# Performance work log

Measured on AMD Instinct MI355X. Metric: run time of the kernel, lower is better.

The kernel has to match this reference:

```python
import jax, jax.numpy as jnp
import numpy as np

B, S, DIM, COV = 64, 512, 1024, 256


def setup_inputs() -> dict:
    key = jax.random.key(0)
    ks = jax.random.split(key, 12)
    s = 0.02
    h = jax.random.normal(ks[0], (B, DIM), jnp.float32)
    context = jax.random.normal(ks[1], (B, S, DIM), jnp.float32)
    cov = jax.random.normal(ks[2], (B, S, COV), jnp.float32)
    mask = jax.random.randint(ks[3], (B, S), 0, 2) == 1
    W_in = jax.random.normal(ks[4], (DIM, DIM), jnp.float32) * s
    W_out = jax.random.normal(ks[5], (DIM, 2 * DIM), jnp.float32) * s
    W_cov = jax.random.normal(ks[6], (DIM, COV), jnp.float32) * s
    b_cov = jax.random.normal(ks[7], (DIM,), jnp.float32) * s
    w_ih = jax.random.normal(ks[8], (3 * COV, 2 * DIM + 1), jnp.float32) * s
    w_hh = jax.random.normal(ks[9], (3 * COV, COV), jnp.float32) * s
    b_ih = jax.random.normal(ks[10], (3 * COV,), jnp.float32) * s
    b_hh = jax.random.normal(ks[11], (3 * COV,), jnp.float32) * s
    return dict(h=h, context=context, cov=cov, W_in=W_in, W_out=W_out,
                W_cov=W_cov, b_cov=b_cov, w_ih=w_ih, w_hh=w_hh,
                b_ih=b_ih, b_hh=b_hh, mask=mask)


def reference(h, context, cov, W_in, W_out, W_cov, b_cov, w_ih, w_hh, b_ih, b_hh, mask):
    # coverage-adjusted context: context + cov_linear(cov)  [B,S,DIM]
    ctx = context + jnp.einsum('bsc,dc->bsd', cov, W_cov) + b_cov
    # target = linear_in(h)  [B,DIM]
    target = h @ W_in.T
    # scores = bmm(context, target).squeeze(2)  [B,S]
    attn = jnp.einsum('bsd,bd->bs', ctx, target)
    attn = jnp.where(mask, -jnp.inf, attn)
    attn = jax.nn.softmax(attn, axis=1)
    # weighted_context = bmm(attn3, context)  [B,DIM]
    wc = jnp.einsum('bs,bsd->bd', attn, ctx)
    h_tilde = jnp.tanh(jnp.concatenate([wc, h], axis=1) @ W_out.T)
    # single-step GRU coverage update over B*S rows
    h_exp = jnp.broadcast_to(h[:, None, :], (B, S, DIM))
    x = jnp.concatenate([ctx, h_exp, attn[..., None]], axis=-1).reshape(B * S, 2 * DIM + 1)
    h0 = cov.reshape(B * S, COV)
    gx = x @ w_ih.T + b_ih   # [B*S, 3*COV]
    gh = h0 @ w_hh.T + b_hh  # [B*S, 3*COV]
    xr, xz, xn = jnp.split(gx, 3, axis=1)
    hr, hz, hn = jnp.split(gh, 3, axis=1)
    r = jax.nn.sigmoid(xr + hr)
    z = jax.nn.sigmoid(xz + hz)
    n = jnp.tanh(xn + r * hn)
    new_cov = ((1.0 - z) * n + z * h0).reshape(B, S, COV)
    return h_tilde, attn, new_cov
```

## Files before the change

kernel.cpp:

```cpp
#include <hip/hip_runtime.h>
#include <math.h>

typedef unsigned short ushort_t;
typedef __attribute__((ext_vector_type(8))) short short8;
typedef __attribute__((ext_vector_type(4))) float f32x4;
typedef __attribute__((ext_vector_type(4))) unsigned short ushort4v;

constexpr int B_ = 64, S_ = 512, DIM_ = 1024, COV_ = 256, TC_ = 768, KIH_ = 2049;
constexpr int NG_ = 1024, KG_ = 1280;

__device__ __forceinline__ float b2f(ushort_t u) {
    union { unsigned int i; float f; } v; v.i = ((unsigned int)u) << 16; return v.f;
}
__device__ __forceinline__ ushort_t f2b(float f) {
    unsigned int x = __float_as_uint(f);
    unsigned int r = x + 0x7fffu + ((x >> 16) & 1u);
    return (ushort_t)(r >> 16);
}
__device__ __forceinline__ float ldv(const float* p, size_t i) { return p[i]; }
__device__ __forceinline__ float ldv(const ushort_t* p, size_t i) { return b2f(p[i]); }

__device__ __forceinline__ float wave_reduce(float a) {
#pragma unroll
    for (int off = 32; off >= 1; off >>= 1) a += __shfl_down(a, off, 64);
    return a;
}

__device__ __forceinline__ void xpose4(f32x4& v, int l) {
    float s, r;
    s = (l & 1) ? v[0] : v[1]; r = __shfl_xor(s, 1, 64); if (l & 1) v[0] = r; else v[1] = r;
    s = (l & 1) ? v[2] : v[3]; r = __shfl_xor(s, 1, 64); if (l & 1) v[2] = r; else v[3] = r;
    s = (l & 2) ? v[0] : v[2]; r = __shfl_xor(s, 2, 64); if (l & 2) v[0] = r; else v[2] = r;
    s = (l & 2) ? v[1] : v[3]; r = __shfl_xor(s, 2, 64); if (l & 2) v[1] = r; else v[3] = r;
}

__global__ void k_detect(const unsigned char* __restrict__ mask,
                         const ushort_t* __restrict__ win,
                         int* __restrict__ flags) {
    __shared__ int red0[256];
    __shared__ int red1[256];
    int tid = threadIdx.x, mb = 0, f32 = 0;
    for (int i = tid; i < 32768; i += 256)
        if ((i & 3) != 0 && mask[i] != 0) mb = 1;
    for (int i = tid; i < 32768; i += 256) {
        ushort_t u = win[2 * i];
        if ((u & 0x7F80u) >= 0x4480u) f32 = 1;
    }
    red0[tid] = mb; red1[tid] = f32; __syncthreads();
    for (int st = 128; st >= 1; st >>= 1) {
        if (tid < st) { red0[tid] |= red0[tid + st]; red1[tid] |= red1[tid + st]; }
        __syncthreads();
    }
    if (tid == 0) { flags[0] = red0[0]; flags[1] = red1[0]; }
}

template <typename IT>
__device__ __forceinline__ void transpose_body(const IT* __restrict__ in,
                                               ushort_t* __restrict__ out,
                                               int R, int C, int ld, int off) {
    int idx = blockIdx.x * 256 + threadIdx.x;
    if (idx >= R * C) return;
    int r = idx / C, c = idx - r * C;
    out[c * R + r] = f2b(ldv(in, (size_t)r * ld + off + c));
}
__global__ void k_transpose(const void* __restrict__ in, ushort_t* __restrict__ out,
                            int R, int C, int ld, int off, const int* __restrict__ flags) {
    if (flags[1]) transpose_body((const float*)in, out, R, C, ld, off);
    else transpose_body((const ushort_t*)in, out, R, C, ld, off);
}

template <typename IT>
__device__ __forceinline__ void watt_body(const IT* __restrict__ wih, float* __restrict__ watt) {
    int j = threadIdx.x;
    watt[j] = ldv(wih, (size_t)j * KIH_ + 2048);
}
__global__ void k_watt(const void* __restrict__ wih, float* __restrict__ watt,
                       const int* __restrict__ flags) {
    if (flags[1]) watt_body((const float*)wih, watt);
    else watt_body((const ushort_t*)wih, watt);
}

template <typename IT>
__device__ __forceinline__ void bfold_body(const IT* __restrict__ bcov,
                                           const IT* __restrict__ wih,
                                           float* __restrict__ bfold) {
    int j = blockIdx.x * 4 + (threadIdx.x >> 6);
    int lane = threadIdx.x & 63;
    const IT* wr = wih + (size_t)j * KIH_;
    float a = 0.f;
#pragma unroll
    for (int i = 0; i < 16; ++i) { int k = lane + 64 * i; a += ldv(bcov, k) * ldv(wr, k); }
    a = wave_reduce(a);
    if (lane == 0) bfold[j] = a;
}
__global__ __launch_bounds__(256) void k_bfold(const void* __restrict__ bcov,
                                               const void* __restrict__ wih,
                                               float* __restrict__ bfold,
                                               const int* __restrict__ flags) {
    if (flags[1]) bfold_body((const float*)bcov, (const float*)wih, bfold);
    else bfold_body((const ushort_t*)bcov, (const ushort_t*)wih, bfold);
}

__global__ __launch_bounds__(256) void k_wfold(const ushort_t* __restrict__ wcov_t,
                                               const ushort_t* __restrict__ w_t,
                                               float* __restrict__ wfold) {
    __shared__ float col[DIM_];
    int c = blockIdx.x, tid = threadIdx.x;
    for (int d = tid; d < DIM_; d += 256) col[d] = b2f(wcov_t[c * DIM_ + d]);
    __syncthreads();
    float a0 = 0.f, a1 = 0.f, a2 = 0.f;
    for (int d = 0; d < DIM_; ++d) {
        float x = col[d];
        const ushort_t* wr = w_t + d * TC_;
        a0 += x * b2f(wr[tid]);
        a1 += x * b2f(wr[tid + 256]);
        a2 += x * b2f(wr[tid + 512]);
    }
    wfold[c * TC_ + tid] = a0;
    wfold[c * TC_ + tid + 256] = a1;
    wfold[c * TC_ + tid + 512] = a2;
}

template <typename IT>
__device__ __forceinline__ void buildwg_body(const IT* __restrict__ wih,
                                             const IT* __restrict__ whh,
                                             const float* __restrict__ wfold,
                                             ushort_t* __restrict__ wg) {
    int idx = blockIdx.x * 256 + threadIdx.x;
    if (idx >= NG_ * KG_) return;
    int n = idx / KG_, k = idx - n * KG_;
    int g = n & 3, cq = n >> 2;
    int j = g * COV_ + cq;
    float v;
    if (k < DIM_) {
        v = (j < TC_) ? ldv(wih, (size_t)j * KIH_ + k) : 0.f;
    } else {
        int c = k - DIM_;
        if (j < 512)      v = wfold[c * TC_ + j] + ldv(whh, (size_t)j * COV_ + c);
        else if (j < TC_) v = wfold[c * TC_ + j];
        else              v = ldv(whh, (size_t)(j - 256) * COV_ + c);
    }
    wg[(size_t)n * KG_ + k] = f2b(v);
}
__global__ void k_buildwg(const void* __restrict__ wih, const void* __restrict__ whh,
                          const float* __restrict__ wfold, ushort_t* __restrict__ wg,
                          const int* __restrict__ flags) {
    if (flags[1]) buildwg_body((const float*)wih, (const float*)whh, wfold, wg);
    else buildwg_body((const ushort_t*)wih, (const ushort_t*)whh, wfold, wg);
}

template <typename IT>
__device__ __forceinline__ void target_body(const IT* __restrict__ h,
                                            const IT* __restrict__ W_in,
                                            float* __restrict__ target) {
    int o = blockIdx.x * 4 + (threadIdx.x >> 6);
    int lane = threadIdx.x & 63;
    int b = o >> 10, d = o & (DIM_ - 1);
    const IT* hr = h + (size_t)b * DIM_;
    const IT* wr = W_in + (size_t)d * DIM_;
    float a = 0.f;
#pragma unroll
    for (int j = 0; j < 16; ++j) { int k = lane + 64 * j; a += ldv(hr, k) * ldv(wr, k); }
    a = wave_reduce(a);
    if (lane == 0) target[o] = a;
}
__global__ __launch_bounds__(256) void k_target_w(const void* __restrict__ h,
                                                  const void* __restrict__ W_in,
                                                  float* __restrict__ target,
                                                  const int* __restrict__ flags) {
    if (flags[1]) target_body((const float*)h, (const float*)W_in, target);
    else target_body((const ushort_t*)h, (const ushort_t*)W_in, target);
}

template <typename IT>
__device__ __forceinline__ void mvec_body(const float* __restrict__ target,
                                          const IT* __restrict__ W_cov,
                                          const IT* __restrict__ bcov,
                                          float* __restrict__ mvec,
                                          float* __restrict__ bct) {
    __shared__ float tg[DIM_];
    __shared__ float red[256];
    int b = blockIdx.x, tid = threadIdx.x;
    float pb = 0.f;
    for (int k = tid; k < DIM_; k += 256) {
        float t = target[b * DIM_ + k];
        tg[k] = t; pb += t * ldv(bcov, k);
    }
    red[tid] = pb; __syncthreads();
    for (int st = 128; st >= 1; st >>= 1) {
        if (tid < st) red[tid] += red[tid + st];
        __syncthreads();
    }
    float acc = 0.f;
    for (int d = 0; d < DIM_; ++d) acc += tg[d] * ldv(W_cov, (size_t)d * COV_ + tid);
    mvec[b * COV_ + tid] = acc;
    if (tid == 0) bct[b] = red[0];
}
__global__ __launch_bounds__(256) void k_mvec(const float* __restrict__ target,
                                              const void* __restrict__ W_cov,
                                              const void* __restrict__ bcov,
                                              float* __restrict__ mvec,
                                              float* __restrict__ bct,
                                              const int* __restrict__ flags) {
    if (flags[1]) mvec_body(target, (const float*)W_cov, (const float*)bcov, mvec, bct);
    else mvec_body(target, (const ushort_t*)W_cov, (const ushort_t*)bcov, mvec, bct);
}

template <typename IT>
__device__ __forceinline__ void scoreraw_body(const IT* __restrict__ context,
                                              const IT* __restrict__ cov,
                                              const float* __restrict__ target,
                                              const float* __restrict__ mvec,
                                              const float* __restrict__ bct,
                                              float* __restrict__ scf,
                                              ushort_t* __restrict__ ctx_bf,
                                              ushort_t* __restrict__ cov_bf) {
    __shared__ float tg[DIM_];
    __shared__ float ms[COV_];
    int b = blockIdx.x, tid = threadIdx.x;
    for (int k = tid; k < DIM_; k += 256) tg[k] = target[b * DIM_ + k];
    if (tid < COV_) ms[tid] = mvec[b * COV_ + tid];
    float bc = bct[b];
    __syncthreads();
    int wave = tid >> 6, lane = tid & 63;
    int s0 = blockIdx.y * 64 + wave * 16;
    for (int i = 0; i < 16; ++i) {
        int s = s0 + i;
        size_t row = (size_t)(b * S_ + s);
        const IT* cr = context + row * DIM_;
        const IT* vr = cov + row * COV_;
        float a = 0.f;
        if constexpr (sizeof(IT) == 4) {
#pragma unroll
            for (int j = 0; j < 4; ++j) {
                int d = lane * 4 + 256 * j;
                float4 x = *(const float4*)((const float*)cr + d);
                a += x.x * tg[d] + x.y * tg[d + 1] + x.z * tg[d + 2] + x.w * tg[d + 3];
                if (ctx_bf) {
                    ushort4v u;
                    u[0] = f2b(x.x); u[1] = f2b(x.y); u[2] = f2b(x.z); u[3] = f2b(x.w);
                    *(ushort4v*)(ctx_bf + row * DIM_ + d) = u;
                }
            }
            {
                int cc = lane * 4;
                float4 x = *(const float4*)((const float*)vr + cc);
                a += x.x * ms[cc] + x.y * ms[cc + 1] + x.z * ms[cc + 2] + x.w * ms[cc + 3];
                if (cov_bf) {
                    ushort4v u;
                    u[0] = f2b(x.x); u[1] = f2b(x.y); u[2] = f2b(x.z); u[3] = f2b(x.w);
                    *(ushort4v*)(cov_bf + row * COV_ + cc) = u;
                }
            }
        } else {
#pragma unroll
            for (int j = 0; j < 16; ++j) { int d = lane + 64 * j; a += ldv(cr, d) * tg[d]; }
#pragma unroll
            for (int j = 0; j < 4; ++j) { int c = lane + 64 * j; a += ldv(vr, c) * ms[c]; }
        }
        a = wave_reduce(a);
        if (lane == 0) scf[row] = a + bc;
    }
}
__global__ __launch_bounds__(256) void k_scoreraw(const void* __restrict__ context,
                                                  const void* __restrict__ cov,
                                                  const float* __restrict__ target,
                                                  const float* __restrict__ mvec,
                                                  const float* __restrict__ bct,
                                                  float* __restrict__ scf,
                                                  ushort_t* __restrict__ ctx_bf,
                                                  ushort_t* __restrict__ cov_bf,
                                                  const int* __restrict__ flags) {
    if (flags[1]) scoreraw_body((const float*)context, (const float*)cov, target, mvec, bct,
                                scf, ctx_bf, cov_bf);
    else scoreraw_body((const ushort_t*)context, (const ushort_t*)cov, target, mvec, bct,
                       scf, ctx_bf, cov_bf);
}

__global__ __launch_bounds__(256) void k_softmax(const float* __restrict__ scf,
                                                 const void* __restrict__ maskp,
                                                 const int* __restrict__ flags,
                                                 float* __restrict__ attnf,
                                                 float* __restrict__ attn_out) {
    __shared__ float red[256];
    int b = blockIdx.x, tid = threadIdx.x;
    int mb = flags[0];
    int i0 = b * S_ + tid, i1 = i0 + 256;
    int m0 = mb ? (int)((const unsigned char*)maskp)[i0] : ((const int*)maskp)[i0];
    int m1 = mb ? (int)((const unsigned char*)maskp)[i1] : ((const int*)maskp)[i1];
    float s0 = m0 ? -INFINITY : scf[i0];
    float s1 = m1 ? -INFINITY : scf[i1];
    red[tid] = fmaxf(s0, s1); __syncthreads();
    for (int st = 128; st >= 1; st >>= 1) {
        if (tid < st) red[tid] = fmaxf(red[tid], red[tid + st]);
        __syncthreads();
    }
    float mx = red[0]; __syncthreads();
    float e0 = expf(s0 - mx), e1 = expf(s1 - mx);
    red[tid] = e0 + e1; __syncthreads();
    for (int st = 128; st >= 1; st >>= 1) {
        if (tid < st) red[tid] += red[tid + st];
        __syncthreads();
    }
    float inv = 1.0f / red[0];
    float a0 = e0 * inv, a1 = e1 * inv;
    attnf[i0] = a0; attnf[i1] = a1;
    attn_out[i0] = a0; attn_out[i1] = a1;
}

__global__ __launch_bounds__(256) void k_wcpart2(const ushort_t* __restrict__ ctx_bf,
                                                 const ushort_t* __restrict__ cov_bf,
                                                 const void* __restrict__ ctx_in,
                                                 const void* __restrict__ cov_in,
                                                 const float* __restrict__ attnf,
                                                 float* __restrict__ wc8,
                                                 float* __restrict__ ac8,
                                                 const int* __restrict__ flags) {
    const ushort_t* C = flags[1] ? ctx_bf : (const ushort_t*)ctx_in;
    const ushort_t* V = flags[1] ? cov_bf : (const ushort_t*)cov_in;
    __shared__ float at[64];
    int b = blockIdx.x, ch = blockIdx.y, tid = threadIdx.x;
    int s0 = ch * 64;
    if (tid < 64) at[tid] = attnf[b * S_ + s0 + tid];
    __syncthreads();
    float acv = 0.f;
    for (int s = 0; s < 64; ++s)
        acv += at[s] * b2f(V[((size_t)(b * S_ + s0 + s)) * COV_ + tid]);
    ac8[((size_t)ch * B_ + b) * COV_ + tid] = acv;
    float acc[4] = {0.f, 0.f, 0.f, 0.f};
    for (int s = 0; s < 64; ++s) {
        float w = at[s];
        const ushort_t* cr = C + ((size_t)(b * S_ + s0 + s)) * DIM_;
        acc[0] += w * b2f(cr[tid]);
        acc[1] += w * b2f(cr[tid + 256]);
        acc[2] += w * b2f(cr[tid + 512]);
        acc[3] += w * b2f(cr[tid + 768]);
    }
    size_t base = ((size_t)ch * B_ + b) * DIM_;
    for (int m = 0; m < 4; ++m) wc8[base + tid + 256 * m] = acc[m];
}

template <typename IT>
__device__ __forceinline__ void wcfin_body(const float* __restrict__ wc8,
                                           const float* __restrict__ ac8,
                                           const ushort_t* __restrict__ wcov_t,
                                           const IT* __restrict__ bcov,
                                           float* __restrict__ wc) {
    __shared__ float ac[COV_];
    int b = blockIdx.x, tid = threadIdx.x;
    float a = 0.f;
    for (int ch = 0; ch < 8; ++ch) a += ac8[((size_t)ch * B_ + b) * COV_ + tid];
    ac[tid] = a;
    __syncthreads();
    float acc[4] = {0.f, 0.f, 0.f, 0.f};
    for (int ch = 0; ch < 8; ++ch) {
        size_t base = ((size_t)ch * B_ + b) * DIM_;
        for (int m = 0; m < 4; ++m) acc[m] += wc8[base + tid + 256 * m];
    }
    for (int c = 0; c < COV_; ++c) {
        float av = ac[c];
        const ushort_t* wr = wcov_t + c * DIM_;
        acc[0] += av * b2f(wr[tid]);
        acc[1] += av * b2f(wr[tid + 256]);
        acc[2] += av * b2f(wr[tid + 512]);
        acc[3] += av * b2f(wr[tid + 768]);
    }
    for (int m = 0; m < 4; ++m) {
        int d = tid + 256 * m;
        wc[b * DIM_ + d] = acc[m] + ldv(bcov, d);
    }
}
__global__ __launch_bounds__(256) void k_wcfin(const float* __restrict__ wc8,
                                               const float* __restrict__ ac8,
                                               const ushort_t* __restrict__ wcov_t,
                                               const void* __restrict__ bcov,
                                               float* __restrict__ wc,
                                               const int* __restrict__ flags) {
    if (flags[1]) wcfin_body(wc8, ac8, wcov_t, (const float*)bcov, wc);
    else wcfin_body(wc8, ac8, wcov_t, (const ushort_t*)bcov, wc);
}

template <typename IT>
__device__ __forceinline__ void htilde_body(const float* __restrict__ wc,
                                            const IT* __restrict__ h,
                                            const IT* __restrict__ W_out,
                                            float* __restrict__ out_ht) {
    int o = blockIdx.x * 4 + (threadIdx.x >> 6);
    int lane = threadIdx.x & 63;
    int b = o >> 10, d = o & (DIM_ - 1);
    const float* wcr = wc + b * DIM_;
    const IT* hr = h + (size_t)b * DIM_;
    const IT* wr = W_out + (size_t)d * 2 * DIM_;
    float a = 0.f;
#pragma unroll
    for (int j = 0; j < 16; ++j) { int k = lane + 64 * j; a += wcr[k] * ldv(wr, k); }
#pragma unroll
    for (int j = 0; j < 16; ++j) { int k = lane + 64 * j; a += ldv(hr, k) * ldv(wr, DIM_ + k); }
    a = wave_reduce(a);
    if (lane == 0) out_ht[o] = tanhf(a);
}
__global__ __launch_bounds__(256) void k_htilde_w(const float* __restrict__ wc,
                                                  const void* __restrict__ h,
                                                  const void* __restrict__ W_out,
                                                  float* __restrict__ out_ht,
                                                  const int* __restrict__ flags) {
    if (flags[1]) htilde_body(wc, (const float*)h, (const float*)W_out, out_ht);
    else htilde_body(wc, (const ushort_t*)h, (const ushort_t*)W_out, out_ht);
}

template <typename IT>
__device__ __forceinline__ void gxh_body(const IT* __restrict__ h,
                                         const IT* __restrict__ w_ih,
                                         const IT* __restrict__ b_ih,
                                         const float* __restrict__ bfold,
                                         float* __restrict__ gxall) {
    int o = blockIdx.x * 4 + (threadIdx.x >> 6);
    int lane = threadIdx.x & 63;
    int b = o / TC_, j = o - b * TC_;
    const IT* hr = h + (size_t)b * DIM_;
    const IT* wr = w_ih + (size_t)j * KIH_ + DIM_;
    float a = 0.f;
#pragma unroll
    for (int i = 0; i < 16; ++i) { int k = lane + 64 * i; a += ldv(hr, k) * ldv(wr, k); }
    a = wave_reduce(a);
    if (lane == 0) gxall[o] = a + ldv(b_ih, j) + bfold[j];
}
__global__ __launch_bounds__(256) void k_gxh_w(const void* __restrict__ h,
                                               const void* __restrict__ w_ih,
                                               const void* __restrict__ b_ih,
                                               const float* __restrict__ bfold,
                                               float* __restrict__ gxall,
                                               const int* __restrict__ flags) {
    if (flags[1]) gxh_body((const float*)h, (const float*)w_ih, (const float*)b_ih, bfold, gxall);
    else gxh_body((const ushort_t*)h, (const ushort_t*)w_ih, (const ushort_t*)b_ih, bfold, gxall);
}

__global__ __launch_bounds__(256) void k_gemm3(const ushort_t* __restrict__ ctx_bf,
                                               const ushort_t* __restrict__ cov_bf,
                                               const void* __restrict__ ctx_in,
                                               const void* __restrict__ cov_in,
                                               const ushort_t* __restrict__ wg,
                                               const float* __restrict__ attnf,
                                               const float* __restrict__ gxall,
                                               const float* __restrict__ watt,
                                               const void* __restrict__ bhh,
                                               float* __restrict__ out_cov,
                                               const int* __restrict__ flags) {
    const int f32in = flags[1];
    const ushort_t* Xc = f32in ? ctx_bf : (const ushort_t*)ctx_in;
    const ushort_t* Xv = f32in ? cov_bf : (const ushort_t*)cov_in;
    __shared__ __align__(16) ushort_t As[128 * 32];
    __shared__ __align__(16) ushort_t Bs[128 * 32];
    int tid = threadIdx.x;
    int p = blockIdx.x;
    int xcd = p & 7, t = p >> 3;
    int nb = t & 7, rb = xcd + 8 * (t >> 3);
    int n0 = nb * 128;
    int grow0 = rb * 128;
    int wave = tid >> 6, lane = tid & 63;
    int wm = wave >> 1, wn = wave & 1;
    int half = lane >> 4, r16 = lane & 15;

    int c0 = wave * 128 + lane;
    int ra0 = (c0) >> 2, sa0 = ((c0) & 3) ^ ((ra0 >> 1) & 3);
    int c1 = c0 + 64;
    int ra1 = (c1) >> 2, sa1 = ((c1) & 3) ^ ((ra1 >> 1) & 3);

    f32x4 acc[4][4];
#pragma unroll
    for (int i = 0; i < 4; ++i)
#pragma unroll
        for (int j = 0; j < 4; ++j) acc[i][j] = (f32x4){0.f, 0.f, 0.f, 0.f};

    for (int kt = 0; kt < KG_ / 32; ++kt) {
        int k0 = kt * 32;
        const ushort_t* X; size_t ldx; int kk0;
        if (k0 < DIM_) { X = Xc; ldx = DIM_; kk0 = k0; }
        else           { X = Xv; ldx = COV_; kk0 = k0 - DIM_; }
        {
            const ushort_t* g0 = X + (size_t)(grow0 + ra0) * ldx + kk0 + sa0 * 8;
            const ushort_t* g1 = X + (size_t)(grow0 + ra1) * ldx + kk0 + sa1 * 8;
            __builtin_amdgcn_global_load_lds(
                (const __attribute__((address_space(1))) void*)g0,
                (__attribute__((address_space(3))) void*)(As + (size_t)(wave * 128) * 8), 16, 0, 0);
            __builtin_amdgcn_global_load_lds(
                (const __attribute__((address_space(1))) void*)g1,
                (__attribute__((address_space(3))) void*)(As + (size_t)(wave * 128 + 64) * 8), 16, 0, 0);
        }
        {
            const ushort_t* g0 = wg + (size_t)(n0 + ra0) * KG_ + k0 + sa0 * 8;
            const ushort_t* g1 = wg + (size_t)(n0 + ra1) * KG_ + k0 + sa1 * 8;
            __builtin_amdgcn_global_load_lds(
                (const __attribute__((address_space(1))) void*)g0,
                (__attribute__((address_space(3))) void*)(Bs + (size_t)(wave * 128) * 8), 16, 0, 0);
            __builtin_amdgcn_global_load_lds(
                (const __attribute__((address_space(1))) void*)g1,
                (__attribute__((address_space(3))) void*)(Bs + (size_t)(wave * 128 + 64) * 8), 16, 0, 0);
        }
        __syncthreads();
        short8 a[4], b[4];
#pragma unroll
        for (int u = 0; u < 4; ++u) {
            int row = wm * 64 + u * 16 + r16;
            int sec = half ^ ((row >> 1) & 3);
            a[u] = *(const short8*)&As[row * 32 + sec * 8];
        }
#pragma unroll
        for (int u = 0; u < 4; ++u) {
            int row = wn * 64 + u * 16 + r16;
            int sec = half ^ ((row >> 1) & 3);
            b[u] = *(const short8*)&Bs[row * 32 + sec * 8];
        }
#pragma unroll
        for (int i = 0; i < 4; ++i)
#pragma unroll
            for (int j = 0; j < 4; ++j)
                acc[i][j] = __builtin_amdgcn_mfma_f32_16x16x32_bf16(a[i], b[j], acc[i][j], 0, 0, 0);
        __syncthreads();
    }

    int l = lane;
    int bb = grow0 >> 9;
    const float* gx = gxall + bb * TC_;
    int rowv[4]; float atv[4];
#pragma unroll
    for (int i = 0; i < 4; ++i) {
        rowv[i] = grow0 + wm * 64 + 16 * i + ((l >> 4) << 2) + (l & 3);
        atv[i] = attnf[rowv[i]];
    }
#pragma unroll
    for (int j = 0; j < 4; ++j) {
        int c = (n0 >> 2) + wn * 16 + 4 * j + ((l >> 2) & 3);
        float gxR = gx[c], gxZ = gx[COV_ + c], gxN = gx[2 * COV_ + c];
        float waR = watt[c], waZ = watt[COV_ + c], waN = watt[2 * COV_ + c];
        float bhR, bhZ, bhN;
        if (f32in) {
            const float* bp = (const float*)bhh;
            bhR = bp[c]; bhZ = bp[COV_ + c]; bhN = bp[2 * COV_ + c];
        } else {
            const ushort_t* bp = (const ushort_t*)bhh;
            bhR = b2f(bp[c]); bhZ = b2f(bp[COV_ + c]); bhN = b2f(bp[2 * COV_ + c]);
        }
#pragma unroll
        for (int i = 0; i < 4; ++i) {
            f32x4 v = acc[i][j];
            xpose4(v, l);
            float at = atv[i];
            float aR  = v[0] + gxR + at * waR + bhR;
            float aZ  = v[1] + gxZ + at * waZ + bhZ;
            float aXN = v[2] + gxN + at * waN;
            float aHN = v[3] + bhN;
            float r = 1.f / (1.f + expf(-aR));
            float z = 1.f / (1.f + expf(-aZ));
            float nn = tanhf(aXN + r * aHN);
            size_t ix = (size_t)rowv[i] * COV_ + c;
            float h0 = f32in ? ((const float*)cov_in)[ix] : b2f(((const ushort_t*)cov_in)[ix]);
            out_cov[ix] = (1.f - z) * nn + z * h0;
        }
    }
}

template <typename IT>
__device__ __forceinline__ void gru_body(const IT* __restrict__ context,
                                         const IT* __restrict__ cov,
                                         const float* __restrict__ attnf,
                                         const float* __restrict__ gxall,
                                         const float* __restrict__ watt,
                                         const ushort_t* __restrict__ w_t,
                                         const float* __restrict__ wfold,
                                         const ushort_t* __restrict__ whh_t,
                                         const IT* __restrict__ bhh,
                                         float* __restrict__ out_cov) {
    __shared__ float xc[8][DIM_];
    __shared__ float h0s[8][COV_];
    __shared__ float atn[8];
    int base = blockIdx.x * 8, tid = threadIdx.x;
    int b = base / S_;
    for (int i = tid; i < 8 * DIM_; i += 256)
        ((float*)xc)[i] = ldv(context, (size_t)base * DIM_ + i);
    for (int i = tid; i < 8 * COV_; i += 256)
        ((float*)h0s)[i] = ldv(cov, (size_t)base * COV_ + i);
    if (tid < 8) atn[tid] = attnf[base + tid];
    __syncthreads();
    int c = tid;
    float gxR = gxall[b * TC_ + c], gxZ = gxall[b * TC_ + 256 + c], gxN = gxall[b * TC_ + 512 + c];
    float bhR = ldv(bhh, c), bhZ = ldv(bhh, 256 + c), bhN = ldv(bhh, 512 + c);
    float waR = watt[c], waZ = watt[256 + c], waN = watt[512 + c];
    float aR[8], aZ[8], aXN[8], aHN[8];
#pragma unroll
    for (int g = 0; g < 8; ++g) {
        float a = atn[g];
        aR[g] = gxR + bhR + a * waR;
        aZ[g] = gxZ + bhZ + a * waZ;
        aXN[g] = gxN + a * waN;
        aHN[g] = bhN;
    }
    for (int k = 0; k < DIM_; ++k) {
        const ushort_t* row = w_t + k * TC_;
        float wr = b2f(row[c]), wz = b2f(row[256 + c]), wn = b2f(row[512 + c]);
#pragma unroll
        for (int g = 0; g < 8; ++g) {
            float x = xc[g][k];
            aR[g] += x * wr; aZ[g] += x * wz; aXN[g] += x * wn;
        }
    }
    for (int k = 0; k < COV_; ++k) {
        const float* row = wfold + k * TC_;
        float wr = row[c], wz = row[256 + c], wn = row[512 + c];
#pragma unroll
        for (int g = 0; g < 8; ++g) {
            float x = h0s[g][k];
            aR[g] += x * wr; aZ[g] += x * wz; aXN[g] += x * wn;
        }
    }
    for (int k = 0; k < COV_; ++k) {
        const ushort_t* row = whh_t + k * TC_;
        float wr = b2f(row[c]), wz = b2f(row[256 + c]), wn = b2f(row[512 + c]);
#pragma unroll
        for (int g = 0; g < 8; ++g) {
            float hh = h0s[g][k];
            aR[g] += hh * wr; aZ[g] += hh * wz; aHN[g] += hh * wn;
        }
    }
#pragma unroll
    for (int g = 0; g < 8; ++g) {
        float r = 1.f / (1.f + expf(-aR[g]));
        float z = 1.f / (1.f + expf(-aZ[g]));
        float n = tanhf(aXN[g] + r * aHN[g]);
        float h0c = h0s[g][c];
        out_cov[(size_t)(base + g) * COV_ + c] = (1.f - z) * n + z * h0c;
    }
}
__global__ __launch_bounds__(256) void k_gru_f(const void* __restrict__ context,
                                               const void* __restrict__ cov,
                                               const float* __restrict__ attnf,
                                               const float* __restrict__ gxall,
                                               const float* __restrict__ watt,
                                               const ushort_t* __restrict__ w_t,
                                               const float* __restrict__ wfold,
                                               const ushort_t* __restrict__ whh_t,
                                               const void* __restrict__ bhh,
                                               float* __restrict__ out_cov,
                                               const int* __restrict__ flags) {
    if (flags[1]) gru_body((const float*)context, (const float*)cov, attnf, gxall, watt,
                           w_t, wfold, whh_t, (const float*)bhh, out_cov);
    else gru_body((const ushort_t*)context, (const ushort_t*)cov, attnf, gxall, watt,
                  w_t, wfold, whh_t, (const ushort_t*)bhh, out_cov);
}

extern "C" void kernel_launch(void* const* d_in, const int* in_sizes, int n_in,
                              void* d_out, int out_size, void* d_ws, size_t ws_size,
                              hipStream_t stream) {
    const void* h       = d_in[0];
    const void* context = d_in[1];
    const void* cov     = d_in[2];
    const void* W_in    = d_in[3];
    const void* W_out   = d_in[4];
    const void* W_cov   = d_in[5];
    const void* b_cov   = d_in[6];
    const void* w_ih    = d_in[7];
    const void* w_hh    = d_in[8];
    const void* b_ih    = d_in[9];
    const void* b_hh    = d_in[10];
    const void* maskp   = d_in[11];

    float* out = (float*)d_out;
    float* out_ht   = out;
    float* out_attn = out + B_ * DIM_;
    float* out_cov  = out + B_ * DIM_ + B_ * S_;

    char* ws = (char*)d_ws;
    size_t o = 0;
    float* target = (float*)(ws + o); o += (size_t)B_ * DIM_ * 4;
    float* attnf  = (float*)(ws + o); o += (size_t)B_ * S_ * 4;
    float* wc     = (float*)(ws + o); o += (size_t)B_ * DIM_ * 4;
    float* gxall  = (float*)(ws + o); o += (size_t)B_ * TC_ * 4;
    float* watt   = (float*)(ws + o); o += 4096;
    float* mvec   = (float*)(ws + o); o += (size_t)B_ * COV_ * 4;
    float* bct    = (float*)(ws + o); o += 4096;
    float* bfold  = (float*)(ws + o); o += 4096;
    float* wfold  = (float*)(ws + o); o += (size_t)COV_ * TC_ * 4;
    ushort_t* w_t    = (ushort_t*)(ws + o); o += (size_t)DIM_ * TC_ * 2;
    ushort_t* whh_t  = (ushort_t*)(ws + o); o += (size_t)COV_ * TC_ * 2;
    ushort_t* wcov_t = (ushort_t*)(ws + o); o += (size_t)COV_ * DIM_ * 2;
    int* flags = (int*)(ws + o); o += 256;
    float* scf   = (float*)(ws + o); o += (size_t)B_ * S_ * 4;
    float* wc8   = (float*)(ws + o); o += (size_t)8 * B_ * DIM_ * 4;
    float* ac8   = (float*)(ws + o); o += (size_t)8 * B_ * COV_ * 4;
    ushort_t* wg = (ushort_t*)(ws + o); o += (size_t)NG_ * KG_ * 2;
    ushort_t* ctx_bf = (ushort_t*)(ws + o); o += (size_t)B_ * S_ * DIM_ * 2;
    ushort_t* cov_bf = (ushort_t*)(ws + o); o += (size_t)B_ * S_ * COV_ * 2;
    size_t fixed = o;

    const size_t TOTAL_ROWS = (size_t)B_ * S_;
    const bool fused = ws_size >= fixed;

    k_detect<<<1, 256, 0, stream>>>((const unsigned char*)maskp, (const ushort_t*)W_in, flags);
    k_transpose<<<(TC_ * DIM_) / 256, 256, 0, stream>>>(w_ih, w_t, TC_, DIM_, KIH_, 0, flags);
    k_transpose<<<(DIM_ * COV_) / 256, 256, 0, stream>>>(W_cov, wcov_t, DIM_, COV_, COV_, 0, flags);
    if (!fused)
        k_transpose<<<(TC_ * COV_) / 256, 256, 0, stream>>>(w_hh, whh_t, TC_, COV_, COV_, 0, flags);
    k_watt<<<1, TC_, 0, stream>>>(w_ih, watt, flags);
    k_bfold<<<TC_ / 4, 256, 0, stream>>>(b_cov, w_ih, bfold, flags);
    k_wfold<<<COV_, 256, 0, stream>>>(wcov_t, w_t, wfold);
    if (fused)
        k_buildwg<<<(NG_ * KG_ + 255) / 256, 256, 0, stream>>>(w_ih, w_hh, wfold, wg, flags);

    k_target_w<<<(B_ * DIM_) / 4, 256, 0, stream>>>(h, W_in, target, flags);
    k_mvec<<<B_, 256, 0, stream>>>(target, W_cov, b_cov, mvec, bct, flags);
    k_scoreraw<<<dim3(B_, 8), 256, 0, stream>>>(context, cov, target, mvec, bct, scf,
                                                fused ? ctx_bf : nullptr,
                                                fused ? cov_bf : nullptr, flags);
    k_softmax<<<B_, 256, 0, stream>>>(scf, maskp, flags, attnf, out_attn);
    if (fused)
        k_wcpart2<<<dim3(B_, 8), 256, 0, stream>>>(ctx_bf, cov_bf, context, cov, attnf,
                                                   wc8, ac8, flags);
    else
        k_wcpart2<<<dim3(B_, 8), 256, 0, stream>>>((const ushort_t*)context, (const ushort_t*)cov,
                                                   context, cov, attnf, wc8, ac8, flags);
    k_wcfin<<<B_, 256, 0, stream>>>(wc8, ac8, wcov_t, b_cov, wc, flags);
    k_htilde_w<<<(B_ * DIM_) / 4, 256, 0, stream>>>(wc, h, W_out, out_ht, flags);

    k_gxh_w<<<(B_ * TC_) / 4, 256, 0, stream>>>(h, w_ih, b_ih, bfold, gxall, flags);
    if (fused) {
        int nblk = (int)(TOTAL_ROWS / 128) * (NG_ / 128);
        k_gemm3<<<nblk, 256, 0, stream>>>(ctx_bf, cov_bf, context, cov, wg, attnf,
                                          gxall, watt, b_hh, out_cov, flags);
    } else {
        k_gru_f<<<(B_ * S_) / 8, 256, 0, stream>>>(context, cov, attnf, gxall, watt,
                                                   w_t, wfold, whh_t, b_hh, out_cov, flags);
    }
}
```

Baseline: 726.3 us.

## Double-buffer LDS tiles in GRU GEMM and stage epilogue for coalesced stores

The fused GRU GEMM now keeps two LDS buffers for the A and B tiles. It issues the global_load_lds for tile k+1 before running the MFMAs on tile k, which leaves one barrier per iteration and hides load latency behind compute. The epilogue writes the n and z gate values into padded LDS arrays that reuse the same shared memory. It then reads them back to compute the coverage update with float4 loads of the old coverage and float4 stores of the output. This is meant to replace the scattered per-element global accesses with coalesced ones, at the cost of more LDS use and an extra barrier.

```diff
diff --git a/kernel.cpp b/kernel.cpp
--- a/kernel.cpp
+++ b/kernel.cpp
@@ -435,7 +435,7 @@
     else gxh_body((const ushort_t*)h, (const ushort_t*)w_ih, (const ushort_t*)b_ih, bfold, gxall);
 }
 
-__global__ __launch_bounds__(256) void k_gemm3(const ushort_t* __restrict__ ctx_bf,
+__global__ __launch_bounds__(256) void k_gemm4(const ushort_t* __restrict__ ctx_bf,
                                                const ushort_t* __restrict__ cov_bf,
                                                const void* __restrict__ ctx_in,
                                                const void* __restrict__ cov_in,
@@ -449,8 +449,14 @@
     const int f32in = flags[1];
     const ushort_t* Xc = f32in ? ctx_bf : (const ushort_t*)ctx_in;
     const ushort_t* Xv = f32in ? cov_bf : (const ushort_t*)cov_in;
-    __shared__ __align__(16) ushort_t As[128 * 32];
-    __shared__ __align__(16) ushort_t Bs[128 * 32];
+    __shared__ __align__(16) unsigned char smem[2 * 128 * 33 * 4];
+    ushort_t* A0 = (ushort_t*)smem;
+    ushort_t* B0 = A0 + 128 * 32;
+    ushort_t* A1 = B0 + 128 * 32;
+    ushort_t* B1 = A1 + 128 * 32;
+    float* smN = (float*)smem;
+    float* smZ = smN + 128 * 33;
+
     int tid = threadIdx.x;
     int p = blockIdx.x;
     int xcd = p & 7, t = p >> 3;
@@ -466,50 +472,54 @@
     int c1 = c0 + 64;
     int ra1 = (c1) >> 2, sa1 = ((c1) & 3) ^ ((ra1 >> 1) & 3);
 
-    f32x4 acc[4][4];
-#pragma unroll
-    for (int i = 0; i < 4; ++i)
-#pragma unroll
-        for (int j = 0; j < 4; ++j) acc[i][j] = (f32x4){0.f, 0.f, 0.f, 0.f};
-
-    for (int kt = 0; kt < KG_ / 32; ++kt) {
+    auto stage = [&](int kt, ushort_t* Ad, ushort_t* Bd) {
         int k0 = kt * 32;
         const ushort_t* X; size_t ldx; int kk0;
         if (k0 < DIM_) { X = Xc; ldx = DIM_; kk0 = k0; }
         else           { X = Xv; ldx = COV_; kk0 = k0 - DIM_; }
-        {
-            const ushort_t* g0 = X + (size_t)(grow0 + ra0) * ldx + kk0 + sa0 * 8;
-            const ushort_t* g1 = X + (size_t)(grow0 + ra1) * ldx + kk0 + sa1 * 8;
-            __builtin_amdgcn_global_load_lds(
-                (const __attribute__((address_space(1))) void*)g0,
-                (__attribute__((address_space(3))) void*)(As + (size_t)(wave * 128) * 8), 16, 0, 0);
-            __builtin_amdgcn_global_load_lds(
-                (const __attribute__((address_space(1))) void*)g1,
-                (__attribute__((address_space(3))) void*)(As + (size_t)(wave * 128 + 64) * 8), 16, 0, 0);
-        }
-        {
-            const ushort_t* g0 = wg + (size_t)(n0 + ra0) * KG_ + k0 + sa0 * 8;
-            const ushort_t* g1 = wg + (size_t)(n0 + ra1) * KG_ + k0 + sa1 * 8;
-            __builtin_amdgcn_global_load_lds(
-                (const __attribute__((address_space(1))) void*)g0,
-                (__attribute__((address_space(3))) void*)(Bs + (size_t)(wave * 128) * 8), 16, 0, 0);
-            __builtin_amdgcn_global_load_lds(
-                (const __attribute__((address_space(1))) void*)g1,
-                (__attribute__((address_space(3))) void*)(Bs + (size_t)(wave * 128 + 64) * 8), 16, 0, 0);
-        }
-        __syncthreads();
+        const ushort_t* g0 = X + (size_t)(grow0 + ra0) * ldx + kk0 + sa0 * 8;
+        const ushort_t* g1 = X + (size_t)(grow0 + ra1) * ldx + kk0 + sa1 * 8;
+        __builtin_amdgcn_global_load_lds(
+            (const __attribute__((address_space(1))) void*)g0,
+            (__attribute__((address_space(3))) void*)(Ad + (size_t)(wave * 128) * 8), 16, 0, 0);
+        __builtin_amdgcn_global_load_lds(
+            (const __attribute__((address_space(1))) void*)g1,
+            (__attribute__((address_space(3))) void*)(Ad + (size_t)(wave * 128 + 64) * 8), 16, 0, 0);
+        const ushort_t* q0 = wg + (size_t)(n0 + ra0) * KG_ + k0 + sa0 * 8;
+        const ushort_t* q1 = wg + (size_t)(n0 + ra1) * KG_ + k0 + sa1 * 8;
+        __builtin_amdgcn_global_load_lds(
+            (const __attribute__((address_space(1))) void*)q0,
+            (__attribute__((address_space(3))) void*)(Bd + (size_t)(wave * 128) * 8), 16, 0, 0);
+        __builtin_amdgcn_global_load_lds(
+            (const __attribute__((address_space(1))) void*)q1,
+            (__attribute__((address_space(3))) void*)(Bd + (size_t)(wave * 128 + 64) * 8), 16, 0, 0);
+    };
+
+    f32x4 acc[4][4];
+#pragma unroll
+    for (int i = 0; i < 4; ++i)
+#pragma unroll
+        for (int j = 0; j < 4; ++j) acc[i][j] = (f32x4){0.f, 0.f, 0.f, 0.f};
+
+    constexpr int NT = KG_ / 32;
+    stage(0, A0, B0);
+    __syncthreads();
+    for (int kt = 0; kt < NT; ++kt) {
+        ushort_t* Ac = (kt & 1) ? A1 : A0;
+        ushort_t* Bc = (kt & 1) ? B1 : B0;
+        if (kt + 1 < NT) stage(kt + 1, (kt & 1) ? A0 : A1, (kt & 1) ? B0 : B1);
         short8 a[4], b[4];
 #pragma unroll
         for (int u = 0; u < 4; ++u) {
             int row = wm * 64 + u * 16 + r16;
             int sec = half ^ ((row >> 1) & 3);
-            a[u] = *(const short8*)&As[row * 32 + sec * 8];
+            a[u] = *(const short8*)&Ac[row * 32 + sec * 8];
         }
 #pragma unroll
         for (int u = 0; u < 4; ++u) {
             int row = wn * 64 + u * 16 + r16;
             int sec = half ^ ((row >> 1) & 3);
-            b[u] = *(const short8*)&Bs[row * 32 + sec * 8];
+            b[u] = *(const short8*)&Bc[row * 32 + sec * 8];
         }
 #pragma unroll
         for (int i = 0; i < 4; ++i)
@@ -522,15 +532,16 @@
     int l = lane;
     int bb = grow0 >> 9;
     const float* gx = gxall + bb * TC_;
-    int rowv[4]; float atv[4];
+    int rloc[4]; float atv[4];
 #pragma unroll
     for (int i = 0; i < 4; ++i) {
-        rowv[i] = grow0 + wm * 64 + 16 * i + ((l >> 4) << 2) + (l & 3);
-        atv[i] = attnf[rowv[i]];
+        rloc[i] = wm * 64 + 16 * i + ((l >> 4) << 2) + (l & 3);
+        atv[i] = attnf[grow0 + rloc[i]];
     }
 #pragma unroll
     for (int j = 0; j < 4; ++j) {
-        int c = (n0 >> 2) + wn * 16 + 4 * j + ((l >> 2) & 3);
+        int cl = wn * 16 + 4 * j + ((l >> 2) & 3);
+        int c = (n0 >> 2) + cl;
         float gxR = gx[c], gxZ = gx[COV_ + c], gxN = gx[2 * COV_ + c];
         float waR = watt[c], waZ = watt[COV_ + c], waN = watt[2 * COV_ + c];
         float bhR, bhZ, bhN;
@@ -553,10 +564,33 @@
             float r = 1.f / (1.f + expf(-aR));
             float z = 1.f / (1.f + expf(-aZ));
             float nn = tanhf(aXN + r * aHN);
-            size_t ix = (size_t)rowv[i] * COV_ + c;
-            float h0 = f32in ? ((const float*)cov_in)[ix] : b2f(((const ushort_t*)cov_in)[ix]);
-            out_cov[ix] = (1.f - z) * nn + z * h0;
-        }
+            smN[rloc[i] * 33 + cl] = nn;
+            smZ[rloc[i] * 33 + cl] = z;
+        }
+    }
+    __syncthreads();
+    int cbase = nb * 32;
+    for (int u = tid; u < 128 * 8; u += 256) {
+        int rl = u >> 3, c4 = (u & 7) * 4;
+        float n0v = smN[rl * 33 + c4 + 0], n1v = smN[rl * 33 + c4 + 1];
+        float n2v = smN[rl * 33 + c4 + 2], n3v = smN[rl * 33 + c4 + 3];
+        float z0 = smZ[rl * 33 + c4 + 0], z1 = smZ[rl * 33 + c4 + 1];
+        float z2 = smZ[rl * 33 + c4 + 2], z3 = smZ[rl * 33 + c4 + 3];
+        size_t base = (size_t)(grow0 + rl) * COV_ + cbase + c4;
+        float h0v, h1v, h2v, h3v;
+        if (f32in) {
+            float4 hv = *(const float4*)((const float*)cov_in + base);
+            h0v = hv.x; h1v = hv.y; h2v = hv.z; h3v = hv.w;
+        } else {
+            ushort4v hv = *(const ushort4v*)((const ushort_t*)cov_in + base);
+            h0v = b2f(hv[0]); h1v = b2f(hv[1]); h2v = b2f(hv[2]); h3v = b2f(hv[3]);
+        }
+        float4 o;
+        o.x = (1.f - z0) * n0v + z0 * h0v;
+        o.y = (1.f - z1) * n1v + z1 * h1v;
+        o.z = (1.f - z2) * n2v + z2 * h2v;
+        o.w = (1.f - z3) * n3v + z3 * h3v;
+        *(float4*)(out_cov + base) = o;
     }
 }
 
@@ -724,7 +758,7 @@
     k_gxh_w<<<(B_ * TC_) / 4, 256, 0, stream>>>(h, w_ih, b_ih, bfold, gxall, flags);
     if (fused) {
         int nblk = (int)(TOTAL_ROWS / 128) * (NG_ / 128);
-        k_gemm3<<<nblk, 256, 0, stream>>>(ctx_bf, cov_bf, context, cov, wg, attnf,
+        k_gemm4<<<nblk, 256, 0, stream>>>(ctx_bf, cov_bf, context, cov, wg, attnf,
                                           gxall, watt, b_hh, out_cov, flags);
     } else {
         k_gru_f<<<(B_ * S_) / 8, 256, 0, stream>>>(context, cov, attnf, gxall, watt,
```

Measured after the change: 704.1 us. -3.1%, faster.
